# Kernel optimization log

Measured on AMD Instinct MI355X. Metric: run time of the kernel, lower is better.

Reference implementation:

```python
import jax, jax.numpy as jnp
import numpy as np

HALF_LOG_2PI = 0.5 * float(np.log(2.0 * np.pi))  # Normal log_prob constant

N_SAMPLES = 33554432  # 32M Monte Carlo samples


def setup_inputs() -> dict:
    key = jax.random.key(0)
    k1, k2 = jax.random.split(key)
    # z1 ~ N(0,1) plays the role of Normal(0,1).sample();
    # z2 ~ N(0,1) is the standardized Normal(3,1).sample() (mean added in reference)
    z1 = jax.random.normal(k1, (N_SAMPLES,), dtype=jnp.float32)
    z2 = jax.random.normal(k2, (N_SAMPLES,), dtype=jnp.float32)
    return {"z1": z1, "z2": z2}


def reference(z1, z2):
    # rnd() = Normal(0,1).sample() + Normal(3,1).sample() = z1 + (3 + z2)
    mu = z1 + z2 + jnp.float32(3.0)
    # Normal(mu, 1).log_prob(0.4) = -0.5*(0.4 - mu)^2 - 0.5*log(2*pi)
    log_likes = -0.5 * jnp.square(jnp.float32(0.4) - mu) - jnp.float32(HALF_LOG_2PI)
    # loss = reduce_mean(reduce_mean(log_likes)) = mean over samples
    return jnp.mean(log_likes)
```

## Files before the change

kernel.cpp:

```cpp
#include <hip/hip_runtime.h>
#include <math.h>

#define N_BLOCKS 2048
#define N_THREADS 256

__global__ void __launch_bounds__(N_THREADS)
partial_sumsq_kernel(const float4* __restrict__ z1,
                     const float4* __restrict__ z2,
                     float* __restrict__ partials,
                     int n4) {
    int tid = blockIdx.x * blockDim.x + threadIdx.x;
    int stride = gridDim.x * blockDim.x;

    float acc = 0.0f;
    for (int i = tid; i < n4; i += stride) {
        float4 a = z1[i];
        float4 b = z2[i];
        float t0 = a.x + b.x + 2.6f;
        float t1 = a.y + b.y + 2.6f;
        float t2 = a.z + b.z + 2.6f;
        float t3 = a.w + b.w + 2.6f;
        acc += t0 * t0 + t1 * t1 + t2 * t2 + t3 * t3;
    }

    #pragma unroll
    for (int off = 32; off > 0; off >>= 1)
        acc += __shfl_down(acc, off, 64);

    __shared__ float wave_sums[N_THREADS / 64];
    int lane = threadIdx.x & 63;
    int wave = threadIdx.x >> 6;
    if (lane == 0) wave_sums[wave] = acc;
    __syncthreads();

    if (threadIdx.x == 0) {
        float s = 0.0f;
        #pragma unroll
        for (int w = 0; w < N_THREADS / 64; ++w) s += wave_sums[w];
        partials[blockIdx.x] = s;
    }
}

__global__ void __launch_bounds__(N_THREADS)
final_reduce_kernel(const float* __restrict__ partials,
                    int nparts,
                    float* __restrict__ out,
                    double inv_n) {
    double acc = 0.0;
    for (int i = threadIdx.x; i < nparts; i += blockDim.x)
        acc += (double)partials[i];

    #pragma unroll
    for (int off = 32; off > 0; off >>= 1)
        acc += __shfl_down(acc, off, 64);

    __shared__ double wave_sums[N_THREADS / 64];
    int lane = threadIdx.x & 63;
    int wave = threadIdx.x >> 6;
    if (lane == 0) wave_sums[wave] = acc;
    __syncthreads();

    if (threadIdx.x == 0) {
        double s = 0.0;
        #pragma unroll
        for (int w = 0; w < N_THREADS / 64; ++w) s += wave_sums[w];
        out[0] = (float)(-0.5 * s * inv_n - 0.91893853320467274178);
    }
}

extern "C" void kernel_launch(void* const* d_in, const int* in_sizes, int n_in,
                              void* d_out, int out_size, void* d_ws, size_t ws_size,
                              hipStream_t stream) {
    const float4* z1 = (const float4*)d_in[0];
    const float4* z2 = (const float4*)d_in[1];
    float* out = (float*)d_out;
    float* partials = (float*)d_ws;

    int n = in_sizes[0];
    int n4 = n / 4;

    partial_sumsq_kernel<<<N_BLOCKS, N_THREADS, 0, stream>>>(z1, z2, partials, n4);
    final_reduce_kernel<<<1, N_THREADS, 0, stream>>>(partials, N_BLOCKS, out,
                                                     1.0 / (double)n);
}
```

Baseline: 49.55 us.

## Fuse final reduction into main kernel via last-block atomic counter and unroll loads

Merges the two-kernel reduction into one launch: each block writes its partial sum, increments a global counter, and the last-arriving block reduces all partials in double and writes the result. The main loop is also unrolled 4x so each thread has more independent float4 loads in flight, and it accumulates with fmaf. This removes a kernel launch and the gap between the kernels, at the cost of an atomic per block and a dependence on the workspace counter, which is never reset and relies on modulo-gridDim wraparound.

```diff
diff --git a/kernel.cpp b/kernel.cpp
--- a/kernel.cpp
+++ b/kernel.cpp
@@ -1,26 +1,55 @@
 #include <hip/hip_runtime.h>
-#include <math.h>
 
 #define N_BLOCKS 2048
 #define N_THREADS 256
 
 __global__ void __launch_bounds__(N_THREADS)
-partial_sumsq_kernel(const float4* __restrict__ z1,
-                     const float4* __restrict__ z2,
-                     float* __restrict__ partials,
-                     int n4) {
-    int tid = blockIdx.x * blockDim.x + threadIdx.x;
-    int stride = gridDim.x * blockDim.x;
+fused_loss_kernel(const float4* __restrict__ z1,
+                  const float4* __restrict__ z2,
+                  float* __restrict__ partials,
+                  unsigned int* __restrict__ counter,
+                  float* __restrict__ out,
+                  int n4, double inv_n) {
+    const int tid = blockIdx.x * blockDim.x + threadIdx.x;
+    const int stride = gridDim.x * blockDim.x;
 
     float acc = 0.0f;
-    for (int i = tid; i < n4; i += stride) {
+    int i = tid;
+    for (; i + 3 * stride < n4; i += 4 * stride) {
+        float4 a0 = z1[i];
+        float4 a1 = z1[i + stride];
+        float4 a2 = z1[i + 2 * stride];
+        float4 a3 = z1[i + 3 * stride];
+        float4 b0 = z2[i];
+        float4 b1 = z2[i + stride];
+        float4 b2 = z2[i + 2 * stride];
+        float4 b3 = z2[i + 3 * stride];
+        float t;
+        t = a0.x + b0.x + 2.6f; acc = fmaf(t, t, acc);
+        t = a0.y + b0.y + 2.6f; acc = fmaf(t, t, acc);
+        t = a0.z + b0.z + 2.6f; acc = fmaf(t, t, acc);
+        t = a0.w + b0.w + 2.6f; acc = fmaf(t, t, acc);
+        t = a1.x + b1.x + 2.6f; acc = fmaf(t, t, acc);
+        t = a1.y + b1.y + 2.6f; acc = fmaf(t, t, acc);
+        t = a1.z + b1.z + 2.6f; acc = fmaf(t, t, acc);
+        t = a1.w + b1.w + 2.6f; acc = fmaf(t, t, acc);
+        t = a2.x + b2.x + 2.6f; acc = fmaf(t, t, acc);
+        t = a2.y + b2.y + 2.6f; acc = fmaf(t, t, acc);
+        t = a2.z + b2.z + 2.6f; acc = fmaf(t, t, acc);
+        t = a2.w + b2.w + 2.6f; acc = fmaf(t, t, acc);
+        t = a3.x + b3.x + 2.6f; acc = fmaf(t, t, acc);
+        t = a3.y + b3.y + 2.6f; acc = fmaf(t, t, acc);
+        t = a3.z + b3.z + 2.6f; acc = fmaf(t, t, acc);
+        t = a3.w + b3.w + 2.6f; acc = fmaf(t, t, acc);
+    }
+    for (; i < n4; i += stride) {
         float4 a = z1[i];
         float4 b = z2[i];
-        float t0 = a.x + b.x + 2.6f;
-        float t1 = a.y + b.y + 2.6f;
-        float t2 = a.z + b.z + 2.6f;
-        float t3 = a.w + b.w + 2.6f;
-        acc += t0 * t0 + t1 * t1 + t2 * t2 + t3 * t3;
+        float t;
+        t = a.x + b.x + 2.6f; acc = fmaf(t, t, acc);
+        t = a.y + b.y + 2.6f; acc = fmaf(t, t, acc);
+        t = a.z + b.z + 2.6f; acc = fmaf(t, t, acc);
+        t = a.w + b.w + 2.6f; acc = fmaf(t, t, acc);
     }
 
     #pragma unroll
@@ -28,43 +57,37 @@
         acc += __shfl_down(acc, off, 64);
 
     __shared__ float wave_sums[N_THREADS / 64];
-    int lane = threadIdx.x & 63;
-    int wave = threadIdx.x >> 6;
+    __shared__ int is_last;
+    const int lane = threadIdx.x & 63;
+    const int wave = threadIdx.x >> 6;
     if (lane == 0) wave_sums[wave] = acc;
     __syncthreads();
 
     if (threadIdx.x == 0) {
-        float s = 0.0f;
-        #pragma unroll
-        for (int w = 0; w < N_THREADS / 64; ++w) s += wave_sums[w];
+        float s = wave_sums[0] + wave_sums[1] + wave_sums[2] + wave_sums[3];
         partials[blockIdx.x] = s;
+        __threadfence();
+        unsigned int old = atomicAdd(counter, 1u);
+        is_last = (((old + 1u) % (unsigned)gridDim.x) == 0u) ? 1 : 0;
     }
-}
-
-__global__ void __launch_bounds__(N_THREADS)
-final_reduce_kernel(const float* __restrict__ partials,
-                    int nparts,
-                    float* __restrict__ out,
-                    double inv_n) {
-    double acc = 0.0;
-    for (int i = threadIdx.x; i < nparts; i += blockDim.x)
-        acc += (double)partials[i];
-
-    #pragma unroll
-    for (int off = 32; off > 0; off >>= 1)
-        acc += __shfl_down(acc, off, 64);
-
-    __shared__ double wave_sums[N_THREADS / 64];
-    int lane = threadIdx.x & 63;
-    int wave = threadIdx.x >> 6;
-    if (lane == 0) wave_sums[wave] = acc;
     __syncthreads();
 
-    if (threadIdx.x == 0) {
-        double s = 0.0;
+    if (is_last) {
+        __threadfence();
+        double d = 0.0;
+        for (int p = threadIdx.x; p < N_BLOCKS; p += N_THREADS)
+            d += (double)__hip_atomic_load(&partials[p], __ATOMIC_RELAXED,
+                                           __HIP_MEMORY_SCOPE_AGENT);
         #pragma unroll
-        for (int w = 0; w < N_THREADS / 64; ++w) s += wave_sums[w];
-        out[0] = (float)(-0.5 * s * inv_n - 0.91893853320467274178);
+        for (int off = 32; off > 0; off >>= 1)
+            d += __shfl_down(d, off, 64);
+        __shared__ double dsum[N_THREADS / 64];
+        if (lane == 0) dsum[wave] = d;
+        __syncthreads();
+        if (threadIdx.x == 0) {
+            double s = dsum[0] + dsum[1] + dsum[2] + dsum[3];
+            out[0] = (float)(-0.5 * s * inv_n - 0.91893853320467274178);
+        }
     }
 }
 
@@ -75,11 +98,11 @@
     const float4* z2 = (const float4*)d_in[1];
     float* out = (float*)d_out;
     float* partials = (float*)d_ws;
+    unsigned int* counter = (unsigned int*)((char*)d_ws + N_BLOCKS * sizeof(float));
 
     int n = in_sizes[0];
     int n4 = n / 4;
 
-    partial_sumsq_kernel<<<N_BLOCKS, N_THREADS, 0, stream>>>(z1, z2, partials, n4);
-    final_reduce_kernel<<<1, N_THREADS, 0, stream>>>(partials, N_BLOCKS, out,
-                                                     1.0 / (double)n);
+    fused_loss_kernel<<<N_BLOCKS, N_THREADS, 0, stream>>>(
+        z1, z2, partials, counter, out, n4, 1.0 / (double)n);
 }
```

Result: slower. 107.8 us (+117.5%).
